# Kernel tuning notes

Hardware: AMD Instinct MI355X
Metric: run time of the kernel (lower is better)

Reference implementation:

```python
import jax, jax.numpy as jnp
import numpy as np

ANCHORS_ALL = np.array([[10.,13.],[16.,30.],[33.,23.],[30.,61.],[62.,45.],
                        [59.,119.],[116.,90.],[156.,198.],[373.,326.]], np.float32)
ANCHORS_MASK = [0, 1, 2]
NUM_CLASS = 80
BBOX_ATTRIB = 5 + NUM_CLASS
IGNORE_THRES = 0.7
EPS = 1e-12


def _iou_cxcywh(a, b):
    ax1, ax2 = a[..., 0] - a[..., 2] / 2, a[..., 0] + a[..., 2] / 2
    ay1, ay2 = a[..., 1] - a[..., 3] / 2, a[..., 1] + a[..., 3] / 2
    bx1, bx2 = b[..., 0] - b[..., 2] / 2, b[..., 0] + b[..., 2] / 2
    by1, by2 = b[..., 1] - b[..., 3] / 2, b[..., 1] + b[..., 3] / 2
    iw = jnp.clip(jnp.minimum(ax2, bx2) - jnp.maximum(ax1, bx1), 0.0)
    ih = jnp.clip(jnp.minimum(ay2, by2) - jnp.maximum(ay1, by1), 0.0)
    inter = iw * ih
    union = a[..., 2] * a[..., 3] + b[..., 2] * b[..., 3] - inter
    return inter / (union + 1e-16)


def _build_targets(pred_boxes, target, anchors_all, anchors, nH, nW):
    # vectorized version of the per-(batch, gt-box) python double loop
    nB, nT, _ = target.shape
    nA = anchors.shape[0]
    # emulate `break` on first all-zero target row via cumulative validity
    valid = jnp.cumprod((target.sum(-1) != 0).astype(jnp.int32), axis=1).astype(bool)  # [B,T]
    gx, gy = target[..., 1] * nW, target[..., 2] * nH
    gw, gh = target[..., 3] * nW, target[..., 4] * nH
    gi = jnp.clip(gx.astype(jnp.int32), 0, nW - 1)
    gj = jnp.clip(gy.astype(jnp.int32), 0, nH - 1)
    gt_boxes = jnp.stack([gx, gy, gw, gh], -1)                                    # [B,T,4]
    # IoU of every GT against every predicted box -> ignore mask for noobj
    ious = _iou_cxcywh(pred_boxes.reshape(nB, 1, -1, 4), gt_boxes[:, :, None, :])  # [B,T,P]
    ignore = (ious > IGNORE_THRES) & valid[..., None]
    noobj_mask = 1.0 - jnp.any(ignore, axis=1).reshape(nB, nA, nH, nW).astype(jnp.float32)
    # anchor matching on w/h only (both boxes centered at origin)
    aw, ah = anchors_all[:, 0], anchors_all[:, 1]                                  # [9]
    inter = jnp.minimum(gw[..., None], aw) * jnp.minimum(gh[..., None], ah)
    union = gw[..., None] * gh[..., None] + aw * ah - inter
    best = jnp.argmax(inter / (union + 1e-16), axis=-1)                            # [B,T]
    lut = -np.ones(len(ANCHORS_ALL), np.int32)
    lut[np.array(ANCHORS_MASK)] = np.arange(nA, dtype=np.int32)
    a_loc = jnp.asarray(lut)[best]
    write = valid & (a_loc >= 0)                # only GTs whose best anchor is in this head's mask
    a_loc = jnp.clip(a_loc, 0)
    b_idx = jnp.where(write, jnp.arange(nB)[:, None], nB)   # route masked-out writes to dummy row nB
    coord_v = jnp.sqrt(2.0 - target[..., 3] * target[..., 4])
    tw_v = jnp.log(gw / anchors[a_loc, 0] + 1e-16)
    th_v = jnp.log(gh / anchors[a_loc, 1] + 1e-16)
    cls_i = jnp.clip(target[..., 0].astype(jnp.int32), 0, NUM_CLASS - 1)

    def scat(vals):
        return jnp.zeros((nB + 1, nA, nH, nW), jnp.float32).at[b_idx, a_loc, gj, gi].set(vals)[:nB]

    obj_mask = scat(jnp.ones_like(gx))
    box_coord_mask = scat(coord_v)
    tx = scat(gx - gi)
    ty = scat(gy - gj)
    tw = scat(tw_v)
    th = scat(th_v)
    tcls = (jnp.zeros((nB + 1, nA, nH, nW, NUM_CLASS), jnp.float32)
            .at[b_idx, a_loc, gj, gi, cls_i].set(1.0)[:nB])
    return obj_mask, noobj_mask, box_coord_mask, obj_mask, tcls, tx, ty, tw, th


def _bce_sum(p, t):
    return -jnp.sum(t * jnp.log(p + EPS) + (1.0 - t) * jnp.log(1.0 - p + EPS))


def _forward(x, target, img_dim):
    nB, _, nH, nW = x.shape
    nA = len(ANCHORS_MASK)
    stride = img_dim / nH
    anchors_all = jnp.asarray(ANCHORS_ALL) / stride
    anchors = anchors_all[jnp.asarray(ANCHORS_MASK)]
    preds = x.reshape(nB, nA, BBOX_ATTRIB, nH, nW).transpose(0, 1, 3, 4, 2)  # [B,A,H,W,85]
    preds_xy = jax.nn.sigmoid(preds[..., :2])
    preds_wh = preds[..., 2:4]
    preds_conf = jax.nn.sigmoid(preds[..., 4])
    preds_cls = jax.nn.sigmoid(preds[..., 5:])
    mesh_xy = jnp.stack(jnp.meshgrid(jnp.arange(nW, dtype=jnp.float32),
                                     jnp.arange(nH, dtype=jnp.float32)), -1)  # [H,W,2] = (x,y)
    # decoded boxes are detached in the original (used only to build targets)
    pred_boxes = jnp.concatenate(
        [jax.lax.stop_gradient(preds_xy) + mesh_xy,
         jnp.exp(jax.lax.stop_gradient(preds_wh)) * anchors[None, :, None, None, :]], -1)
    tgt = jax.lax.stop_gradient(target)  # target.detach() in original
    (obj_mask, noobj_mask, box_coord_mask, tconf, tcls,
     tx, ty, tw, th) = _build_targets(pred_boxes, tgt, anchors_all, anchors, nH, nW)
    mse = lambda a, b: jnp.sum((a - b) ** 2)
    loss_x = mse(preds_xy[..., 0] * box_coord_mask, tx * box_coord_mask) / 2
    loss_y = mse(preds_xy[..., 1] * box_coord_mask, ty * box_coord_mask) / 2
    loss_w = mse(preds_wh[..., 0] * box_coord_mask, tw * box_coord_mask) / 2
    loss_h = mse(preds_wh[..., 1] * box_coord_mask, th * box_coord_mask) / 2
    loss_conf = (_bce_sum(preds_conf * obj_mask, obj_mask)
                 + _bce_sum(preds_conf * noobj_mask, jnp.zeros_like(preds_conf)))
    # BCE over cls entries of object cells only (sum reduction) == mask-weighted sum
    loss_cls = -jnp.sum(obj_mask[..., None] * (tcls * jnp.log(preds_cls + EPS)
                                               + (1.0 - tcls) * jnp.log(1.0 - preds_cls + EPS)))
    return loss_x + loss_y + loss_w + loss_h + loss_conf + loss_cls


def setup_inputs() -> dict:
    key = jax.random.key(0)
    k1, k2, k3, k4 = jax.random.split(key, 4)
    nB, nT = 16, 50
    x = jax.random.normal(k1, (nB, 3 * BBOX_ATTRIB, 76, 76), jnp.float32)
    cls = jnp.floor(jax.random.uniform(k2, (nB, nT, 1)) * NUM_CLASS)
    cxy = jax.random.uniform(k3, (nB, nT, 2), minval=0.05, maxval=0.95)
    wh = jax.random.uniform(k4, (nB, nT, 2), minval=0.02, maxval=0.4)
    target = jnp.concatenate([cls, cxy, wh], -1).astype(jnp.float32)
    return {"x": x, "target": target, "img_dim": 608}


def reference(x, target, img_dim):
    return _forward(x, target, img_dim)
```

## Files before the change

kernel.cpp:

```cpp
#include <hip/hip_runtime.h>

#define NBATCH 16
#define NTGT   50
#define NA     3
#define NH     76
#define NW     76
#define HW     (NH*NW)
#define NC     80
#define NATT   85
#define CELLS  (NA*HW)

__device__ __constant__ float c_anchors[18] = {
  10.f,13.f, 16.f,30.f, 33.f,23.f, 30.f,61.f, 62.f,45.f,
  59.f,119.f, 116.f,90.f, 156.f,198.f, 373.f,326.f };

#define OFF_AREA 3200
#define OFF_NV   4000

__device__ inline float read_dim(const void* p) {
  int iv = *(const int*)p;
  if (iv > 0 && iv < (1 << 24)) return (float)iv;
  return *(const float*)p;
}

__global__ void yolo_prep_obj(const float* __restrict__ tgt,
                              const float* __restrict__ x,
                              const void*  __restrict__ dimp,
                              float*       __restrict__ wsf,
                              float*       __restrict__ out) {
  __shared__ int skey[NTGT];
  __shared__ int scl [NTGT];
  int b = blockIdx.x;
  int t = threadIdx.x;
  float istride = (float)NH / read_dim(dimp);

  float cls = 0.f, cx = 0.f, cy = 0.f, w = 0.f, h = 0.f, s = 1.f;
  if (t < NTGT) {
    const float* tr = tgt + (size_t)(b * NTGT + t) * 5;
    cls = tr[0]; cx = tr[1]; cy = tr[2]; w = tr[3]; h = tr[4];
    s = cls + cx + cy + w + h;
  }
  unsigned long long mz = __ballot(t < NTGT && s == 0.0f);
  int nv = mz ? (__ffsll(mz) - 1) : NTGT;

  float gx = cx * NW, gy = cy * NH, gw = w * NW, gh = h * NH;
  int gi = min(max((int)gx, 0), NW - 1);
  int gj = min(max((int)gy, 0), NH - 1);

  float best_r = -1.0f; int best = 0;
  for (int k = 0; k < 9; k++) {
    float aw = c_anchors[2*k] * istride, ah = c_anchors[2*k+1] * istride;
    float inter = fminf(gw, aw) * fminf(gh, ah);
    float uni   = gw * gh + aw * ah - inter;
    float r = inter / (uni + 1e-16f);
    if (r > best_r) { best_r = r; best = k; }
  }
  int a = (best < NA) ? best : 0;
  int mykey = (t < nv && best < NA) ? (a * HW + gj * NW + gi) : -1;

  if (t < NTGT) {
    skey[t] = mykey;
    scl [t] = min(max((int)cls, 0), NC - 1);
    float4* wbox = (float4*)wsf;
    wbox[b * NTGT + t] = make_float4(gx - gw*0.5f, gx + gw*0.5f,
                                     gy - gh*0.5f, gy + gh*0.5f);
    wsf[OFF_AREA + b * NTGT + t] = gw * gh;
  }
  if (t == 0) ((int*)wsf)[OFF_NV + b] = nv;
  __syncthreads();

  float loss = 0.0f;
  if (mykey >= 0) {
    bool winner = true;
    unsigned cb0 = 0, cb1 = 0, cb2 = 0;
    for (int t2 = 0; t2 < nv; t2++) {
      if (skey[t2] == mykey) {
        if (t2 > t) winner = false;
        int c = scl[t2];
        if (c < 32)      cb0 |= (1u << c);
        else if (c < 64) cb1 |= (1u << (c - 32));
        else             cb2 |= (1u << (c - 64));
      }
    }
    if (winner) {
      const float* xb = x + ((size_t)(b * NA + a) * NATT) * HW + gj * NW + gi;
      float px = xb[0*HW], py = xb[1*HW], pw = xb[2*HW], ph = xb[3*HW], pc = xb[4*HW];
      float spx   = 1.0f / (1.0f + __expf(-px));
      float spy   = 1.0f / (1.0f + __expf(-py));
      float sconf = 1.0f / (1.0f + __expf(-pc));
      float aw = c_anchors[2*a] * istride, ah = c_anchors[2*a+1] * istride;
      loss += -__logf(sconf + 1e-12f);
      float m  = sqrtf(2.0f - w * h);
      float dx = (spx - (gx - (float)gi)) * m;
      float dy = (spy - (gy - (float)gj)) * m;
      float dw = (pw  - __logf(gw / aw + 1e-16f)) * m;
      float dh = (ph  - __logf(gh / ah + 1e-16f)) * m;
      loss += 0.5f * (dx*dx + dy*dy + dw*dw + dh*dh);
      for (int c = 0; c < NC; c++) {
        float pv = 1.0f / (1.0f + __expf(-xb[(5 + c) * HW]));
        bool on = (c < 32) ? ((cb0 >> c) & 1u)
                : (c < 64) ? ((cb1 >> (c - 32)) & 1u)
                           : ((cb2 >> (c - 64)) & 1u);
        loss += on ? -__logf(pv + 1e-12f) : -__logf(1.0f - pv + 1e-12f);
      }
    }
  }
  for (int off = 32; off > 0; off >>= 1) loss += __shfl_down(loss, off, 64);
  if (t == 0) atomicAdd(out, loss);
}

__launch_bounds__(256)
__global__ void yolo_noobj(const float* __restrict__ x,
                           const float* __restrict__ wsf,
                           const void*  __restrict__ dimp,
                           float*       __restrict__ out) {
  __shared__ float4 sbox[NTGT];
  __shared__ float  sarea[NTGT];
  __shared__ int    snv;
  __shared__ float  sred[4];

  int b   = blockIdx.y;
  int tid = threadIdx.x;
  if (tid < NTGT) {
    sbox [tid] = ((const float4*)wsf)[b * NTGT + tid];
    sarea[tid] = wsf[OFF_AREA + b * NTGT + tid];
  }
  if (tid == 0) snv = ((const int*)wsf)[OFF_NV + b];
  __syncthreads();

  float loss = 0.0f;
  int cell = blockIdx.x * blockDim.x + tid;
  if (cell < CELLS) {
    int a   = cell / HW;
    int rem = cell - a * HW;
    int j   = rem / NW;
    int i   = rem - j * NW;
    const float* xb = x + ((size_t)(b * NA + a) * NATT) * HW + rem;
    float px = xb[0*HW], py = xb[1*HW], pw = xb[2*HW], ph = xb[3*HW], pc = xb[4*HW];
    float spx   = 1.0f / (1.0f + __expf(-px));
    float spy   = 1.0f / (1.0f + __expf(-py));
    float sconf = 1.0f / (1.0f + __expf(-pc));
    float istride = (float)NH / read_dim(dimp);
    float bw = __expf(pw) * c_anchors[2*a]   * istride;
    float bh = __expf(ph) * c_anchors[2*a+1] * istride;
    float bx = spx + (float)i, by = spy + (float)j;
    float ax1 = bx - bw * 0.5f, ax2 = bx + bw * 0.5f;
    float ay1 = by - bh * 0.5f, ay2 = by + bh * 0.5f;
    float areaA = bw * bh;

    bool ign = false;
    int nv = snv;
    for (int t = 0; t < nv; t++) {
      float4 bb = sbox[t];
      float iw = fmaxf(fminf(ax2, bb.y) - fmaxf(ax1, bb.x), 0.0f);
      float ih = fmaxf(fminf(ay2, bb.w) - fmaxf(ay1, bb.z), 0.0f);
      float inter = iw * ih;
      float uni   = areaA + sarea[t] - inter + 1e-16f;
      ign = ign | (inter > 0.7f * uni);
    }
    if (!ign) loss += -__logf(1.0f - sconf + 1e-12f);
  }

  for (int off = 32; off > 0; off >>= 1) loss += __shfl_down(loss, off, 64);
  int wave = tid >> 6, lane = tid & 63;
  if (lane == 0) sred[wave] = loss;
  __syncthreads();
  if (tid == 0) atomicAdd(out, sred[0] + sred[1] + sred[2] + sred[3]);
}

extern "C" void kernel_launch(void* const* d_in, const int* in_sizes, int n_in,
                              void* d_out, int out_size, void* d_ws, size_t ws_size,
                              hipStream_t stream) {
  const float* x    = (const float*)d_in[0];
  const float* tgt  = (const float*)d_in[1];
  const void*  dimp = d_in[2];
  float* out = (float*)d_out;
  float* wsf = (float*)d_ws;

  hipMemsetAsync(out, 0, sizeof(float) * out_size, stream);

  yolo_prep_obj<<<NBATCH, 64, 0, stream>>>(tgt, x, dimp, wsf, out);

  dim3 grid((CELLS + 255) / 256, NBATCH);
  yolo_noobj<<<grid, 256, 0, stream>>>(x, wsf, dimp, out);
}
```

Before: 167.7 us.

## Fuse target prep into noobj kernel and replace atomics with deterministic partial reduction

Result: faster. 150.9 us (-10.1%).

```diff
diff --git a/kernel.cpp b/kernel.cpp
--- a/kernel.cpp
+++ b/kernel.cpp
@@ -9,13 +9,13 @@
 #define NC     80
 #define NATT   85
 #define CELLS  (NA*HW)
+#define CBLK   68
+#define BPB    (CBLK + 1)
+#define NPART  (BPB * NBATCH)
 
 __device__ __constant__ float c_anchors[18] = {
   10.f,13.f, 16.f,30.f, 33.f,23.f, 30.f,61.f, 62.f,45.f,
   59.f,119.f, 116.f,90.f, 156.f,198.f, 373.f,326.f };
-
-#define OFF_AREA 3200
-#define OFF_NV   4000
 
 __device__ inline float read_dim(const void* p) {
   int iv = *(const int*)p;
@@ -23,59 +23,100 @@
   return *(const float*)p;
 }
 
-__global__ void yolo_prep_obj(const float* __restrict__ tgt,
-                              const float* __restrict__ x,
-                              const void*  __restrict__ dimp,
-                              float*       __restrict__ wsf,
-                              float*       __restrict__ out) {
-  __shared__ int skey[NTGT];
-  __shared__ int scl [NTGT];
-  int b = blockIdx.x;
-  int t = threadIdx.x;
+__launch_bounds__(256)
+__global__ void yolo_all(const float* __restrict__ x,
+                         const float* __restrict__ tgt,
+                         const void*  __restrict__ dimp,
+                         float*       __restrict__ wsf) {
+  __shared__ float4 sbox[NTGT];
+  __shared__ float  sarea[NTGT];
+  __shared__ int    skey[NTGT];
+  __shared__ int    scl [NTGT];
+  __shared__ int    snv;
+  __shared__ float  sred[4];
+
+  int b   = blockIdx.y;
+  int bx  = blockIdx.x;
+  int tid = threadIdx.x;
   float istride = (float)NH / read_dim(dimp);
 
-  float cls = 0.f, cx = 0.f, cy = 0.f, w = 0.f, h = 0.f, s = 1.f;
-  if (t < NTGT) {
-    const float* tr = tgt + (size_t)(b * NTGT + t) * 5;
-    cls = tr[0]; cx = tr[1]; cy = tr[2]; w = tr[3]; h = tr[4];
-    s = cls + cx + cy + w + h;
+  float gx = 0.f, gy = 0.f, gw = 0.f, gh = 0.f, w = 0.f, h = 0.f;
+  int   gi = 0, gj = 0, a = 0, mykey = -1;
+  if (tid < 64) {
+    float cls = 0.f, cx = 0.f, cy = 0.f, s = 1.f;
+    if (tid < NTGT) {
+      const float* tr = tgt + (size_t)(b * NTGT + tid) * 5;
+      cls = tr[0]; cx = tr[1]; cy = tr[2]; w = tr[3]; h = tr[4];
+      s = cls + cx + cy + w + h;
+    }
+    unsigned long long mz = __ballot(tid < NTGT && s == 0.0f);
+    int nv = mz ? (__ffsll(mz) - 1) : NTGT;
+
+    gx = cx * NW; gy = cy * NH; gw = w * NW; gh = h * NH;
+    gi = min(max((int)gx, 0), NW - 1);
+    gj = min(max((int)gy, 0), NH - 1);
+
+    float best_r = -1.0f; int best = 0;
+    for (int k = 0; k < 9; k++) {
+      float aw = c_anchors[2*k] * istride, ah = c_anchors[2*k+1] * istride;
+      float inter = fminf(gw, aw) * fminf(gh, ah);
+      float uni   = gw * gh + aw * ah - inter;
+      float r = inter / (uni + 1e-16f);
+      if (r > best_r) { best_r = r; best = k; }
+    }
+    a = (best < NA) ? best : 0;
+    mykey = (tid < nv && best < NA) ? (a * HW + gj * NW + gi) : -1;
+
+    if (tid < NTGT) {
+      sbox[tid]  = make_float4(gx - gw*0.5f, gx + gw*0.5f,
+                               gy - gh*0.5f, gy + gh*0.5f);
+      sarea[tid] = gw * gh;
+      skey[tid]  = mykey;
+      scl [tid]  = min(max((int)cls, 0), NC - 1);
+    }
+    if (tid == 0) snv = nv;
   }
-  unsigned long long mz = __ballot(t < NTGT && s == 0.0f);
-  int nv = mz ? (__ffsll(mz) - 1) : NTGT;
-
-  float gx = cx * NW, gy = cy * NH, gw = w * NW, gh = h * NH;
-  int gi = min(max((int)gx, 0), NW - 1);
-  int gj = min(max((int)gy, 0), NH - 1);
-
-  float best_r = -1.0f; int best = 0;
-  for (int k = 0; k < 9; k++) {
-    float aw = c_anchors[2*k] * istride, ah = c_anchors[2*k+1] * istride;
-    float inter = fminf(gw, aw) * fminf(gh, ah);
-    float uni   = gw * gh + aw * ah - inter;
-    float r = inter / (uni + 1e-16f);
-    if (r > best_r) { best_r = r; best = k; }
-  }
-  int a = (best < NA) ? best : 0;
-  int mykey = (t < nv && best < NA) ? (a * HW + gj * NW + gi) : -1;
-
-  if (t < NTGT) {
-    skey[t] = mykey;
-    scl [t] = min(max((int)cls, 0), NC - 1);
-    float4* wbox = (float4*)wsf;
-    wbox[b * NTGT + t] = make_float4(gx - gw*0.5f, gx + gw*0.5f,
-                                     gy - gh*0.5f, gy + gh*0.5f);
-    wsf[OFF_AREA + b * NTGT + t] = gw * gh;
-  }
-  if (t == 0) ((int*)wsf)[OFF_NV + b] = nv;
   __syncthreads();
 
   float loss = 0.0f;
-  if (mykey >= 0) {
+  int nv = snv;
+
+  if (bx < CBLK) {
+    int cell = bx * 256 + tid;
+    if (cell < CELLS) {
+      int ca  = cell / HW;
+      int rem = cell - ca * HW;
+      int j   = rem / NW;
+      int i   = rem - j * NW;
+      const float* xb = x + ((size_t)(b * NA + ca) * NATT) * HW + rem;
+      float px = xb[0*HW], py = xb[1*HW], pw = xb[2*HW], ph = xb[3*HW], pc = xb[4*HW];
+      float spx   = 1.0f / (1.0f + __expf(-px));
+      float spy   = 1.0f / (1.0f + __expf(-py));
+      float sconf = 1.0f / (1.0f + __expf(-pc));
+      float bw = __expf(pw) * c_anchors[2*ca]   * istride;
+      float bh = __expf(ph) * c_anchors[2*ca+1] * istride;
+      float bxc = spx + (float)i, byc = spy + (float)j;
+      float ax1 = bxc - bw * 0.5f, ax2 = bxc + bw * 0.5f;
+      float ay1 = byc - bh * 0.5f, ay2 = byc + bh * 0.5f;
+      float areaA = bw * bh;
+
+      bool ign = false;
+      for (int t = 0; t < nv; t++) {
+        float4 bb = sbox[t];
+        float iw = fmaxf(fminf(ax2, bb.y) - fmaxf(ax1, bb.x), 0.0f);
+        float ih = fmaxf(fminf(ay2, bb.w) - fmaxf(ay1, bb.z), 0.0f);
+        float inter = iw * ih;
+        float uni   = areaA + sarea[t] - inter + 1e-16f;
+        ign = ign | (inter > 0.7f * uni);
+      }
+      if (!ign) loss = -__logf(1.0f - sconf + 1e-12f);
+    }
+  } else if (tid < 64 && mykey >= 0) {
     bool winner = true;
     unsigned cb0 = 0, cb1 = 0, cb2 = 0;
     for (int t2 = 0; t2 < nv; t2++) {
       if (skey[t2] == mykey) {
-        if (t2 > t) winner = false;
+        if (t2 > tid) winner = false;
         int c = scl[t2];
         if (c < 32)      cb0 |= (1u << c);
         else if (c < 64) cb1 |= (1u << (c - 32));
@@ -105,67 +146,25 @@
       }
     }
   }
-  for (int off = 32; off > 0; off >>= 1) loss += __shfl_down(loss, off, 64);
-  if (t == 0) atomicAdd(out, loss);
-}
-
-__launch_bounds__(256)
-__global__ void yolo_noobj(const float* __restrict__ x,
-                           const float* __restrict__ wsf,
-                           const void*  __restrict__ dimp,
-                           float*       __restrict__ out) {
-  __shared__ float4 sbox[NTGT];
-  __shared__ float  sarea[NTGT];
-  __shared__ int    snv;
-  __shared__ float  sred[4];
-
-  int b   = blockIdx.y;
-  int tid = threadIdx.x;
-  if (tid < NTGT) {
-    sbox [tid] = ((const float4*)wsf)[b * NTGT + tid];
-    sarea[tid] = wsf[OFF_AREA + b * NTGT + tid];
-  }
-  if (tid == 0) snv = ((const int*)wsf)[OFF_NV + b];
-  __syncthreads();
-
-  float loss = 0.0f;
-  int cell = blockIdx.x * blockDim.x + tid;
-  if (cell < CELLS) {
-    int a   = cell / HW;
-    int rem = cell - a * HW;
-    int j   = rem / NW;
-    int i   = rem - j * NW;
-    const float* xb = x + ((size_t)(b * NA + a) * NATT) * HW + rem;
-    float px = xb[0*HW], py = xb[1*HW], pw = xb[2*HW], ph = xb[3*HW], pc = xb[4*HW];
-    float spx   = 1.0f / (1.0f + __expf(-px));
-    float spy   = 1.0f / (1.0f + __expf(-py));
-    float sconf = 1.0f / (1.0f + __expf(-pc));
-    float istride = (float)NH / read_dim(dimp);
-    float bw = __expf(pw) * c_anchors[2*a]   * istride;
-    float bh = __expf(ph) * c_anchors[2*a+1] * istride;
-    float bx = spx + (float)i, by = spy + (float)j;
-    float ax1 = bx - bw * 0.5f, ax2 = bx + bw * 0.5f;
-    float ay1 = by - bh * 0.5f, ay2 = by + bh * 0.5f;
-    float areaA = bw * bh;
-
-    bool ign = false;
-    int nv = snv;
-    for (int t = 0; t < nv; t++) {
-      float4 bb = sbox[t];
-      float iw = fmaxf(fminf(ax2, bb.y) - fmaxf(ax1, bb.x), 0.0f);
-      float ih = fmaxf(fminf(ay2, bb.w) - fmaxf(ay1, bb.z), 0.0f);
-      float inter = iw * ih;
-      float uni   = areaA + sarea[t] - inter + 1e-16f;
-      ign = ign | (inter > 0.7f * uni);
-    }
-    if (!ign) loss += -__logf(1.0f - sconf + 1e-12f);
-  }
 
   for (int off = 32; off > 0; off >>= 1) loss += __shfl_down(loss, off, 64);
   int wave = tid >> 6, lane = tid & 63;
   if (lane == 0) sred[wave] = loss;
   __syncthreads();
-  if (tid == 0) atomicAdd(out, sred[0] + sred[1] + sred[2] + sred[3]);
+  if (tid == 0) wsf[b * BPB + bx] = sred[0] + sred[1] + sred[2] + sred[3];
+}
+
+__global__ void yolo_reduce(const float* __restrict__ wsf,
+                            float*       __restrict__ out) {
+  __shared__ float sred[4];
+  int tid = threadIdx.x;
+  float s = 0.0f;
+  for (int i = tid; i < NPART; i += 256) s += wsf[i];
+  for (int off = 32; off > 0; off >>= 1) s += __shfl_down(s, off, 64);
+  int wave = tid >> 6, lane = tid & 63;
+  if (lane == 0) sred[wave] = s;
+  __syncthreads();
+  if (tid == 0) out[0] = sred[0] + sred[1] + sred[2] + sred[3];
 }
 
 extern "C" void kernel_launch(void* const* d_in, const int* in_sizes, int n_in,
@@ -177,10 +176,7 @@
   float* out = (float*)d_out;
   float* wsf = (float*)d_ws;
 
-  hipMemsetAsync(out, 0, sizeof(float) * out_size, stream);
-
-  yolo_prep_obj<<<NBATCH, 64, 0, stream>>>(tgt, x, dimp, wsf, out);
-
-  dim3 grid((CELLS + 255) / 256, NBATCH);
-  yolo_noobj<<<grid, 256, 0, stream>>>(x, wsf, dimp, out);
+  dim3 grid(BPB, NBATCH);
+  yolo_all<<<grid, 256, 0, stream>>>(x, tgt, dimp, wsf);
+  yolo_reduce<<<1, 256, 0, stream>>>(wsf, out);
 }
```
